# Performance work log

Measured on AMD Instinct MI355X. Metric: run time of the kernel, lower is better.

## Reference

```python
import jax, jax.numpy as jnp
from jax import lax
import numpy as np

B, P, G, C = 16, 6000, 128, 10
PC_MIN = np.array([-54.0, -54.0, -5.0], np.float32)
PC_MAX = np.array([54.0, 54.0, 3.0], np.float32)
CENTER_RADIUS = 1.5
CANDIDATE_TOPK = 5
NUM_HEADS = 6
CLS_W, ALPHA, GAMMA = 2.0, 0.25, 2.0
REG_W, IOU_W = 0.25, 0.25
EPS = 1e-12
INF1, INF2 = 10000.0, 100000.0


def _aabb(boxes):
    # boxes: (N,7) [cx,cy,cz,dx,dy,dz,yaw] -> AABB (min,max) of the 8 rotated corners
    c, d, yaw = boxes[:, :3], boxes[:, 3:6], boxes[:, 6]
    ca, sa = jnp.abs(jnp.cos(yaw)), jnp.abs(jnp.sin(yaw))
    hx = 0.5 * (d[:, 0] * ca + d[:, 1] * sa)
    hy = 0.5 * (d[:, 0] * sa + d[:, 1] * ca)
    h = jnp.stack([hx, hy, 0.5 * d[:, 2]], -1)
    return c - h, c + h


def _iou3d(pred7, gt7):
    # axis-aligned 3D IoU over corner AABBs (reference stand-in for rotated BboxOverlaps3D)
    pmin, pmax = _aabb(pred7)
    gmin, gmax = _aabb(gt7)
    lo = jnp.maximum(pmin[:, None], gmin[None])   # (P,G,3)
    hi = jnp.minimum(pmax[:, None], gmax[None])
    inter = jnp.prod(jnp.maximum(hi - lo, 0.0), -1)
    vp = jnp.prod(pmax - pmin, -1)
    vg = jnp.prod(gmax - gmin, -1)
    return inter / (vp[:, None] + vg[None] - inter + 1e-7)


def _cost_matrix(pred_logits, pred_boxes, gt_boxes, gt_labels):
    # --- focal classification cost ---
    p = jax.nn.sigmoid(pred_logits)                                  # (P,C)
    neg = -jnp.log(1.0 - p + EPS) * (1.0 - ALPHA) * p ** GAMMA
    pos = -jnp.log(p + EPS) * ALPHA * (1.0 - p) ** GAMMA
    cls_cost = (pos - neg)[:, gt_labels] * CLS_W                     # (P,G)

    gt_norm = jnp.concatenate([gt_boxes[:, :3], jnp.log(gt_boxes[:, 3:6]),
                               jnp.sin(gt_boxes[:, 6:7]), jnp.cos(gt_boxes[:, 6:7])], -1)  # (G,8)
    reg_cost = jnp.abs(pred_boxes[:, None, :8] - gt_norm[None]).sum(-1) * REG_W

    # --- IoU cost on denormalized pred boxes ---
    yaw = jnp.arctan2(pred_boxes[:, 6], pred_boxes[:, 7])
    pred7 = jnp.concatenate([pred_boxes[:, :3], jnp.exp(pred_boxes[:, 3:6]), yaw[:, None]], -1)
    ious = _iou3d(pred7, gt_boxes)                                   # (P,G)
    iou_cost = -ious * IOU_W

    # --- in-gt-box / in-center geometric prior ---
    ctr = pred_boxes[:, :3]
    gmin, gmax = _aabb(gt_boxes)
    in_box = jnp.all((ctr[:, None] > gmin[None]) & (ctr[:, None] < gmax[None]), -1)  # (P,G)
    gc, gd = gt_boxes[:, :3], gt_boxes[:, 3:6]
    lo = gc - CENTER_RADIUS * gd
    hi = gc + CENTER_RADIUS * gd
    in_ctr = jnp.all((ctr[:, None] > lo[None]) & (ctr[:, None] < hi[None]), -1)
    valid = jnp.any(in_box, 1) | jnp.any(in_ctr, 1)                  # (P,)
    in_both = in_box & in_ctr

    cost = cls_cost + reg_cost + iou_cost + (~in_both).astype(cls_cost.dtype) * 100.0
    cost = cost + (~valid).astype(cls_cost.dtype)[:, None] * INF1
    return cost, ious, valid


def _assign(pred_logits, pred_boxes, gt_boxes, gt_labels, head_idx):
    cost, ious, valid = _cost_matrix(pred_logits, pred_boxes, gt_boxes, gt_labels)

    # dynamic-k per gt: sum of top-k ious minus head-schedule offset, truncated, min 1
    k = min(CANDIDATE_TOPK, P)
    topk_ious = lax.top_k(ious.T, k)[0]                              # (G,k)
    dyn = jnp.maximum((topk_ious.sum(1) - 0.5 * (NUM_HEADS - head_idx)).astype(jnp.int32), 1)

    # per-gt lowest-cost top-dyn selection via double argsort ranks
    ranks = jnp.argsort(jnp.argsort(cost, axis=0), axis=0)           # (P,G)
    matching = (ranks < dyn[None, :]).astype(cost.dtype)

    # priors matched to >1 gt: keep only the min-cost gt
    prior_mask = matching.sum(1) > 1
    onehot_min = jax.nn.one_hot(jnp.argmin(cost, 1), G, dtype=cost.dtype)
    matching = jnp.where(prior_mask[:, None], onehot_min, matching)

    rows = jnp.arange(P)

    def cond(s):
        i, cst, m = s
        return jnp.any(m.sum(0) == 0) & (i < G + 8)

    def body(s):
        i, cst, m = s
        cst = cst + (m.sum(1) > 0).astype(cst.dtype)[:, None] * INF2
        unmatched = m.sum(0) == 0                                    # (G,)
        pos = jnp.argmin(cst, 0)                                     # (G,) best prior per gt
        m = jnp.where((rows[:, None] == pos[None]) & unmatched[None], 1.0, m)
        over = jnp.any(m.sum(1) > 1)
        oh = jax.nn.one_hot(jnp.argmin(cst, 1), G, dtype=cst.dtype)
        m = jnp.where(over & prior_mask[:, None], oh, m)             # stale mask, as in torch source
        return i + 1, cst, m

    _, _, matching = lax.while_loop(cond, body, (jnp.int32(0), cost, matching))

    fg = matching.sum(1) > 0                                         # (P,) foreground mask
    matched = jnp.where(fg, jnp.argmax(matching, 1), -1).astype(jnp.int32)
    return fg, matched


def setup_inputs():
    key = jax.random.key(0)
    k1, k2, k3, k4, k5, k6, k7, k8 = jax.random.split(key, 8)
    pred_logits = jax.random.normal(k1, (B, P, C), jnp.float32)
    ctr = jax.random.uniform(k2, (B, P, 3), jnp.float32, jnp.array(PC_MIN), jnp.array(PC_MAX))
    logsz = jnp.log(jax.random.uniform(k3, (B, P, 3), jnp.float32, 1.0, 4.0))
    ang = jax.random.uniform(k4, (B, P, 1), jnp.float32, -np.pi, np.pi)
    vel = jax.random.normal(k5, (B, P, 2), jnp.float32)
    pred_boxes = jnp.concatenate([ctr, logsz, jnp.sin(ang), jnp.cos(ang), vel], -1)
    gctr = jax.random.uniform(k6, (B, G, 3), jnp.float32, jnp.array(PC_MIN), jnp.array(PC_MAX))
    gsz = jax.random.uniform(k7, (B, G, 3), jnp.float32, 1.0, 5.0)
    gyaw = jax.random.uniform(k8, (B, G, 1), jnp.float32, -np.pi, np.pi)
    gt_boxes = jnp.concatenate([gctr, gsz, gyaw], -1)
    gt_labels = jax.random.randint(jax.random.fold_in(key, 99), (B, G), 0, C)
    return {"pred_logits": pred_logits, "pred_boxes": pred_boxes,
            "gt_boxes": gt_boxes, "gt_labels": gt_labels, "head_idx": 5}


def reference(pred_logits, pred_boxes, gt_boxes, gt_labels, head_idx):
    f = lambda pl, pb, gb, gl: _assign(pl, pb, gb, gl, head_idx)
    fg, matched = jax.vmap(f)(pred_logits, pred_boxes, gt_boxes, gt_labels)
    return fg, matched
```

## Files before the change

kernel.cpp:

```cpp
#include <hip/hip_runtime.h>
#include <stdint.h>
#include <math.h>

#define NB 16
#define NP 6000
#define NG 128
#define NC 10
#define SELMAX 4
#define GSTR 24
#define CPB 2
#define QN 24
#define EPIW 128

typedef unsigned long long u64;
#define NBPs ((size_t)NB * NP)

__device__ __forceinline__ uint32_t fkey(float f) {
  uint32_t u = __float_as_uint(f);
  return (u & 0x80000000u) ? ~u : (u | 0x80000000u);
}
__device__ __forceinline__ float fkey_inv(uint32_t k) {
  uint32_t u = (k & 0x80000000u) ? (k & 0x7fffffffu) : ~k;
  return __uint_as_float(u);
}
__device__ __forceinline__ u64 shfl_xor_u64(u64 v, int m) {
  uint32_t lo = (uint32_t)v, hi = (uint32_t)(v >> 32);
  lo = (uint32_t)__shfl_xor((int)lo, m, 64);
  hi = (uint32_t)__shfl_xor((int)hi, m, 64);
  return ((u64)hi << 32) | lo;
}
__device__ __forceinline__ u64 block_min_u64(u64 v, u64* sred, int lane, int wid) {
  for (int o = 1; o < 64; o <<= 1) {
    u64 t = shfl_xor_u64(v, o);
    if (t < v) v = t;
  }
  __syncthreads();
  if (lane == 0) sred[wid] = v;
  __syncthreads();
  u64 r = sred[0];
  if (sred[1] < r) r = sred[1];
  if (sred[2] < r) r = sred[2];
  if (sred[3] < r) r = sred[3];
  return r;
}

__device__ __forceinline__ void ins5max(uint32_t& a0, uint32_t& a1, uint32_t& a2,
                                        uint32_t& a3, uint32_t& a4, uint32_t k) {
  if (k > a4) {
    a4 = k;
    if (a4 > a3) { uint32_t t = a4; a4 = a3; a3 = t; }
    if (a3 > a2) { uint32_t t = a3; a3 = a2; a2 = t; }
    if (a2 > a1) { uint32_t t = a2; a2 = a1; a1 = t; }
    if (a1 > a0) { uint32_t t = a1; a1 = a0; a0 = t; }
  }
}
__device__ __forceinline__ void ins4min(u64& c0, u64& c1, u64& c2, u64& c3, u64 k) {
  if (k < c3) {
    c3 = k;
    if (c3 < c2) { u64 t = c3; c3 = c2; c2 = t; }
    if (c2 < c1) { u64 t = c2; c2 = c1; c1 = t; }
    if (c1 < c0) { u64 t = c1; c1 = c0; c0 = t; }
  }
}
__device__ __forceinline__ void wave_top5_iou(uint32_t a0, uint32_t a1,
                                              uint32_t a2, uint32_t a3,
                                              uint32_t a4, int lane,
                                              float* dst) {
  int hp = 0;
  for (int k = 0; k < 5; ++k) {
    uint32_t cand = (hp == 0) ? a0 : (hp == 1) ? a1 : (hp == 2) ? a2
                  : (hp == 3) ? a3 : (hp == 4) ? a4 : 0u;
    u64 key = ((u64)cand << 32) | (unsigned)lane;
    u64 r = key;
    for (int o = 1; o < 64; o <<= 1) {
      u64 t = shfl_xor_u64(r, o);
      if (t > r) r = t;
    }
    if (lane == 0) dst[k] = fkey_inv((uint32_t)(r >> 32));
    if (r == key) hp++;
  }
}
__device__ __forceinline__ void wave_top4_cost(u64 c0, u64 c1, u64 c2, u64 c3,
                                               int lane, u64* dst) {
  int hp = 0;
  for (int k = 0; k < 4; ++k) {
    u64 cand = (hp == 0) ? c0 : (hp == 1) ? c1 : (hp == 2) ? c2
             : (hp == 3) ? c3 : ~0ull;
    u64 r = cand;
    for (int o = 1; o < 64; o <<= 1) {
      u64 t = shfl_xor_u64(r, o);
      if (t < r) r = t;
    }
    if (lane == 0) dst[k] = r;
    if (r == cand) hp++;
  }
}

__global__ __launch_bounds__(256) void prep_kernel(
    const float* __restrict__ gt_boxes,
    const int* __restrict__ gt_labels,
    const float* __restrict__ pred_logits,
    const float* __restrict__ pred_boxes,
    float* __restrict__ gtaux,
    float* __restrict__ paux,
    float* __restrict__ clst,
    int* __restrict__ rowcnt,
    int* __restrict__ rowassign,
    int* __restrict__ colcnt,
    int* __restrict__ wcount) {
#pragma clang fp contract(off)
  __shared__ float shg[NG * 12];
  const int b = blockIdx.y, tid = threadIdx.x;
  if (tid < NG) {
    const int g = tid;
    const float* gb = gt_boxes + ((size_t)b * NG + g) * 7;
    float cx = gb[0], cy = gb[1], cz = gb[2];
    float dx = gb[3], dy = gb[4], dz = gb[5];
    float yaw = gb[6];
    float cyw = cosf(yaw), syw = sinf(yaw);
    float ca = fabsf(cyw), sa = fabsf(syw);
    float hx = 0.5f * (dx * ca + dy * sa);
    float hy = 0.5f * (dx * sa + dy * ca);
    float hz = 0.5f * dz;
    float gmin0 = cx - hx, gmin1 = cy - hy, gmin2 = cz - hz;
    float gmax0 = cx + hx, gmax1 = cy + hy, gmax2 = cz + hz;
    float* s = &shg[g * 12];
    s[0] = gmin0; s[1] = gmin1; s[2] = gmin2;
    s[3] = gmax0; s[4] = gmax1; s[5] = gmax2;
    s[6] = cx - 1.5f * dx; s[7] = cy - 1.5f * dy; s[8] = cz - 1.5f * dz;
    s[9] = cx + 1.5f * dx; s[10] = cy + 1.5f * dy; s[11] = cz + 1.5f * dz;
    if (blockIdx.x == 0) {
      float vg = ((gmax0 - gmin0) * (gmax1 - gmin1)) * (gmax2 - gmin2);
      float* o = gtaux + ((size_t)b * NG + g) * GSTR;
      o[0] = gmin0; o[1] = gmin1; o[2] = gmin2;
      o[3] = gmax0; o[4] = gmax1; o[5] = gmax2;
      o[6] = s[6]; o[7] = s[7]; o[8] = s[8];
      o[9] = s[9]; o[10] = s[10]; o[11] = s[11];
      o[12] = cx; o[13] = cy; o[14] = cz;
      o[15] = logf(dx); o[16] = logf(dy); o[17] = logf(dz);
      o[18] = syw; o[19] = cyw;
      o[20] = vg;
      o[21] = __int_as_float(gt_labels[(size_t)b * NG + g]);
      o[22] = 0.0f; o[23] = 0.0f;
      colcnt[b * NG + g] = 0;
      if (b == 0 && g == 0) wcount[0] = 0;
    }
  }
  __syncthreads();
  const int p = blockIdx.x * 256 + tid;
  if (p >= NP) return;
  const size_t idx = (size_t)b * NP + p;
  const float* lg = pred_logits + idx * NC;
  for (int c = 0; c < NC; ++c) {
    float x = lg[c];
    float pr = 1.0f / (1.0f + expf(-x));
    float neg = (-logf(1.0f - pr + 1e-12f) * 0.75f) * (pr * pr);
    float pos = (-logf(pr + 1e-12f) * 0.25f) * ((1.0f - pr) * (1.0f - pr));
    clst[(size_t)c * NBPs + idx] = (pos - neg) * 2.0f;
  }
  const float* bx = pred_boxes + idx * 10;
  float b0 = bx[0], b1 = bx[1], b2 = bx[2], b3 = bx[3], b4 = bx[4];
  float b5 = bx[5], b6 = bx[6], b7 = bx[7];
  float yaw = atan2f(b6, b7);
  float d0 = expf(b3), d1 = expf(b4), d2 = expf(b5);
  float ca = fabsf(cosf(yaw)), sa = fabsf(sinf(yaw));
  float hx = 0.5f * (d0 * ca + d1 * sa);
  float hy = 0.5f * (d0 * sa + d1 * ca);
  float hz = 0.5f * d2;
  float pmin0 = b0 - hx, pmin1 = b1 - hy, pmin2 = b2 - hz;
  float pmax0 = b0 + hx, pmax1 = b1 + hy, pmax2 = b2 + hz;
  int valid = 0;
  for (int g = 0; g < NG; ++g) {
    const float* s = &shg[g * 12];
    bool inb = (b0 > s[0]) && (b0 < s[3]) && (b1 > s[1]) && (b1 < s[4]) &&
               (b2 > s[2]) && (b2 < s[5]);
    bool inc = (b0 > s[6]) && (b0 < s[9]) && (b1 > s[7]) && (b1 < s[10]) &&
               (b2 > s[8]) && (b2 < s[11]);
    if (inb || inc) { valid = 1; break; }
  }
  float* o = paux + idx * 16;
  o[0] = b0; o[1] = b1; o[2] = b2; o[3] = b3;
  o[4] = b4; o[5] = b5; o[6] = b6; o[7] = b7;
  o[8] = pmin0; o[9] = pmin1; o[10] = pmin2;
  o[11] = pmax0; o[12] = pmax1; o[13] = pmax2;
  o[14] = ((pmax0 - pmin0) * (pmax1 - pmin1)) * (pmax2 - pmin2);
  o[15] = valid ? 0.0f : 10000.0f;
  rowcnt[idx] = 0;
  rowassign[idx] = 0x7fffffff;
}

struct GTp {
  float gmin0, gmin1, gmin2, gmax0, gmax1, gmax2;
  float lo0, lo1, lo2, hi0, hi1, hi2;
  float gtn0, gtn1, gtn2, gtn3, gtn4, gtn5, gtn6, gtn7;
  float vg;
  int label;
};
__device__ __forceinline__ GTp load_gt(const float* __restrict__ gtaux,
                                       int b, int g) {
  const float* ga = gtaux + ((size_t)b * NG + g) * GSTR;
  GTp t;
  t.gmin0 = ga[0]; t.gmin1 = ga[1]; t.gmin2 = ga[2];
  t.gmax0 = ga[3]; t.gmax1 = ga[4]; t.gmax2 = ga[5];
  t.lo0 = ga[6]; t.lo1 = ga[7]; t.lo2 = ga[8];
  t.hi0 = ga[9]; t.hi1 = ga[10]; t.hi2 = ga[11];
  t.gtn0 = ga[12]; t.gtn1 = ga[13]; t.gtn2 = ga[14]; t.gtn3 = ga[15];
  t.gtn4 = ga[16]; t.gtn5 = ga[17]; t.gtn6 = ga[18]; t.gtn7 = ga[19];
  t.vg = ga[20];
  t.label = __float_as_int(ga[21]);
  return t;
}

__device__ __forceinline__ float cost_base(
    float b0, float b1, float b2, float b3, float b4, float b5, float b6,
    float b7, float pmin0, float pmin1, float pmin2, float pmax0, float pmax1,
    float pmax2, float vp, float cls, const GTp& t, float* iou_out) {
#pragma clang fp contract(off)
  float r = fabsf(b0 - t.gtn0);
  r = r + fabsf(b1 - t.gtn1);
  r = r + fabsf(b2 - t.gtn2);
  r = r + fabsf(b3 - t.gtn3);
  r = r + fabsf(b4 - t.gtn4);
  r = r + fabsf(b5 - t.gtn5);
  r = r + fabsf(b6 - t.gtn6);
  r = r + fabsf(b7 - t.gtn7);
  float reg = r * 0.25f;
  float li0 = fmaxf(pmin0, t.gmin0), li1 = fmaxf(pmin1, t.gmin1),
        li2 = fmaxf(pmin2, t.gmin2);
  float hj0 = fminf(pmax0, t.gmax0), hj1 = fminf(pmax1, t.gmax1),
        hj2 = fminf(pmax2, t.gmax2);
  float e0 = fmaxf(hj0 - li0, 0.0f), e1 = fmaxf(hj1 - li1, 0.0f),
        e2 = fmaxf(hj2 - li2, 0.0f);
  float inter = (e0 * e1) * e2;
  float iou = inter / (((vp + t.vg) - inter) + 1e-7f);
  bool inb = (b0 > t.gmin0) && (b0 < t.gmax0) && (b1 > t.gmin1) &&
             (b1 < t.gmax1) && (b2 > t.gmin2) && (b2 < t.gmax2);
  bool inc = (b0 > t.lo0) && (b0 < t.hi0) && (b1 > t.lo1) && (b1 < t.hi1) &&
             (b2 > t.lo2) && (b2 < t.hi2);
  *iou_out = iou;
  return ((cls + reg) + (-(iou * 0.25f))) + ((inb && inc) ? 0.0f : 100.0f);
}

__global__ __launch_bounds__(256) void select_kernel(
    const float* __restrict__ paux,
    const float* __restrict__ clst,
    const float* __restrict__ gtaux,
    const int* __restrict__ head_ptr,
    int* __restrict__ colsel,
    int* __restrict__ rowcnt,
    int* __restrict__ rowassign,
    int* __restrict__ wlist,
    int* __restrict__ wcount) {
#pragma clang fp contract(off)
  const int n = blockIdx.x;
  const int orig = (n & 7) * 128 + (n >> 3);
  const int b = orig >> 6;
  const int g0 = (orig & 63) * CPB;
  const int tid = threadIdx.x;
  const int lane = tid & 63, wid = tid >> 6;

  const GTp t0 = load_gt(gtaux, b, g0);
  const GTp t1 = load_gt(gtaux, b, g0 + 1);
  const size_t rowbase = (size_t)b * NP;

  uint32_t i0a = 0, i0b = 0, i0c = 0, i0d = 0, i0e = 0;
  uint32_t i1a = 0, i1b = 0, i1c = 0, i1d = 0, i1e = 0;
  u64 k0a = ~0ull, k0b = ~0ull, k0c = ~0ull, k0d = ~0ull;
  u64 k1a = ~0ull, k1b = ~0ull, k1c = ~0ull, k1d = ~0ull;

  for (int q = 0; q < QN; ++q) {
    const int p = q * 256 + tid;
    if (p < NP) {
      const size_t idx = rowbase + p;
      const float4* pa = (const float4*)(paux + idx * 16);
      float4 A = pa[0], B = pa[1], C = pa[2], D = pa[3];
      float cls0 = clst[(size_t)t0.label * NBPs + idx];
      float cls1 = clst[(size_t)t1.label * NBPs + idx];
      float iou0, iou1;
      float c0 = cost_base(A.x, A.y, A.z, A.w, B.x, B.y, B.z, B.w,
                           C.x, C.y, C.z, C.w, D.x, D.y, D.z,
                           cls0, t0, &iou0);
      float c1 = cost_base(A.x, A.y, A.z, A.w, B.x, B.y, B.z, B.w,
                           C.x, C.y, C.z, C.w, D.x, D.y, D.z,
                           cls1, t1, &iou1);
      ins5max(i0a, i0b, i0c, i0d, i0e, fkey(iou0));
      ins5max(i1a, i1b, i1c, i1d, i1e, fkey(iou1));
      ins4min(k0a, k0b, k0c, k0d, ((u64)fkey(c0 + D.w) << 32) | (unsigned)p);
      ins4min(k1a, k1b, k1c, k1d, ((u64)fkey(c1 + D.w) << 32) | (unsigned)p);
    }
  }

  __shared__ float iouF[4][CPB][5];
  __shared__ u64 ckF[4][CPB][4];
  wave_top5_iou(i0a, i0b, i0c, i0d, i0e, lane, &iouF[wid][0][0]);
  wave_top5_iou(i1a, i1b, i1c, i1d, i1e, lane, &iouF[wid][1][0]);
  wave_top4_cost(k0a, k0b, k0c, k0d, lane, &ckF[wid][0][0]);
  wave_top4_cost(k1a, k1b, k1c, k1d, lane, &ckF[wid][1][0]);
  __syncthreads();

  if (tid < CPB) {
    const int c = tid;
    const int g = g0 + c;
    const int col = b * NG + g;
    float m0 = -INFINITY, m1 = -INFINITY, m2 = -INFINITY, m3 = -INFINITY,
          m4 = -INFINITY;
    for (int w = 0; w < 4; ++w) {
      for (int j = 0; j < 5; ++j) {
        float v = iouF[w][c][j];
        if (v > m4) {
          m4 = v;
          if (m4 > m3) { float t = m4; m4 = m3; m3 = t; }
          if (m3 > m2) { float t = m3; m3 = m2; m2 = t; }
          if (m2 > m1) { float t = m2; m2 = m1; m1 = t; }
          if (m1 > m0) { float t = m1; m1 = m0; m0 = t; }
        }
      }
    }
    float sum5 = ((((m0 + m1) + m2) + m3) + m4);
    float adj = sum5 - 0.5f * (float)(6 - head_ptr[0]);
    int dyn = (int)adj;
    if (dyn < 1) dyn = 1;
    if (dyn > SELMAX) dyn = SELMAX;
    u64 s0 = ~0ull, s1 = ~0ull, s2 = ~0ull, s3 = ~0ull;
    for (int w = 0; w < 4; ++w) {
      for (int j = 0; j < 4; ++j) {
        u64 k = ckF[w][c][j];
        if (k < s3) {
          s3 = k;
          if (s3 < s2) { u64 t = s3; s3 = s2; s2 = t; }
          if (s2 < s1) { u64 t = s2; s2 = s1; s1 = t; }
          if (s1 < s0) { u64 t = s1; s1 = s0; s0 = t; }
        }
      }
    }
    int pk0 = (int)(s0 & 0xffffffffu);
    int pk1 = (int)(s1 & 0xffffffffu);
    int pk2 = (int)(s2 & 0xffffffffu);
    int pk3 = (int)(s3 & 0xffffffffu);
    int sel0 = (dyn > 0) ? pk0 : -1;
    int sel1 = (dyn > 1) ? pk1 : -1;
    int sel2 = (dyn > 2) ? pk2 : -1;
    int sel3 = (dyn > 3) ? pk3 : -1;
    colsel[(size_t)col * SELMAX + 0] = sel0;
    colsel[(size_t)col * SELMAX + 1] = sel1;
    colsel[(size_t)col * SELMAX + 2] = sel2;
    colsel[(size_t)col * SELMAX + 3] = sel3;
    int sels[4] = {sel0, sel1, sel2, sel3};
    for (int k = 0; k < SELMAX; ++k) {
      int sel = sels[k];
      if (sel >= 0) {
        int old = atomicAdd(&rowcnt[rowbase + sel], 1);
        if (old == 1) {
          int slot = atomicAdd(wcount, 1);
          wlist[slot] = (int)(rowbase + sel);
        }
        atomicMin(&rowassign[rowbase + sel], g);
      }
    }
  }
}

__global__ __launch_bounds__(256) void epi_kernel(
    const float* __restrict__ paux,
    const float* __restrict__ clst,
    const float* __restrict__ gtaux,
    const int* __restrict__ colsel,
    const int* __restrict__ rowcnt,
    const int* __restrict__ wlist,
    const int* __restrict__ wcount,
    int* __restrict__ rowminArr,
    int* __restrict__ colcnt) {
#pragma clang fp contract(off)
  const int tid = threadIdx.x;
  if (blockIdx.x >= EPIW) {
    const int col = (blockIdx.x - EPIW) * 256 + tid;
    if (col < NB * NG) {
      const int b = col / NG;
      int cnt = 0;
      const size_t cb = (size_t)col * SELMAX;
      for (int k = 0; k < SELMAX; ++k) {
        int s = colsel[cb + k];
        if (s >= 0 && rowcnt[(size_t)b * NP + s] == 1) cnt++;
      }
      if (cnt) atomicAdd(&colcnt[col], cnt);
    }
    return;
  }
  const int lane = tid & 63, wid = tid >> 6;
  const int wavesTotal = EPIW * 4;
  const int wave = blockIdx.x * 4 + wid;
  const int n = wcount[0];
  for (int e = wave; e < n; e += wavesTotal) {
    const int idx = wlist[e];
    const int b = idx / NP;
    const float4* pa = (const float4*)(paux + (size_t)idx * 16);
    float4 A = pa[0], Bq = pa[1], Cq = pa[2], Dq = pa[3];
    const float pen = Dq.w;
    u64 best = ~0ull;
    for (int h = 0; h < 2; ++h) {
      const int g = h * 64 + lane;
      GTp t = load_gt(gtaux, b, g);
      float cls = clst[(size_t)t.label * NBPs + idx];
      float iou;
      float cc = cost_base(A.x, A.y, A.z, A.w, Bq.x, Bq.y, Bq.z, Bq.w,
                           Cq.x, Cq.y, Cq.z, Cq.w, Dq.x, Dq.y, Dq.z,
                           cls, t, &iou);
      u64 key = ((u64)fkey(cc + pen) << 32) | (unsigned)g;
      if (key < best) best = key;
    }
    for (int o = 1; o < 64; o <<= 1) {
      u64 t = shfl_xor_u64(best, o);
      if (t < best) best = t;
    }
    if (lane == 0) {
      const int bg = (int)(best & 0xffffffffu);
      rowminArr[idx] = bg;
      atomicAdd(&colcnt[b * NG + bg], 1);
    }
  }
}

__global__ __launch_bounds__(256) void fixup_kernel(
    const float* __restrict__ paux,
    const float* __restrict__ clst,
    const float* __restrict__ gtaux,
    const int* __restrict__ colcnt,
    const int* __restrict__ rowcnt,
    int* __restrict__ rowassign) {
#pragma clang fp contract(off)
  const int g = blockIdx.x, b = blockIdx.y, tid = threadIdx.x;
  if (colcnt[b * NG + g] != 0) return;
  const int lane = tid & 63, wid = tid >> 6;
  const size_t rowbase = (size_t)b * NP;
  GTp t = load_gt(gtaux, b, g);
  u64 best = ~0ull;
  for (int p = tid; p < NP; p += 256) {
    const size_t idx = rowbase + p;
    if (rowcnt[idx] == 0) {
      const float4* pa = (const float4*)(paux + idx * 16);
      float4 A = pa[0], Bq = pa[1], Cq = pa[2], Dq = pa[3];
      float cls = clst[(size_t)t.label * NBPs + idx];
      float iou;
      float cc = cost_base(A.x, A.y, A.z, A.w, Bq.x, Bq.y, Bq.z, Bq.w,
                           Cq.x, Cq.y, Cq.z, Cq.w, Dq.x, Dq.y, Dq.z,
                           cls, t, &iou);
      u64 key = ((u64)fkey(cc + Dq.w) << 32) | (unsigned)p;
      if (key < best) best = key;
    }
  }
  __shared__ u64 sred[4];
  u64 rr = block_min_u64(best, sred, lane, wid);
  if (tid == 0) {
    int pos = (int)(rr & 0xffffffffu);
    atomicMin(&rowassign[rowbase + pos], g);
  }
}

__global__ void output_kernel(const int* __restrict__ rowcnt,
                              const int* __restrict__ rowassign,
                              const int* __restrict__ rowminArr,
                              int* __restrict__ out) {
  const int i = blockIdx.x * 256 + threadIdx.x;
  if (i >= (int)NBPs) return;
  int rc = rowcnt[i];
  int fg, m;
  if (rc == 0) {
    int ra = rowassign[i];
    if (ra == 0x7fffffff) { fg = 0; m = -1; }
    else { fg = 1; m = ra; }
  } else if (rc == 1) {
    fg = 1; m = rowassign[i];
  } else {
    fg = 1; m = rowminArr[i];
  }
  out[i] = fg;
  out[NBPs + i] = m;
}

extern "C" void kernel_launch(void* const* d_in, const int* in_sizes, int n_in,
                              void* d_out, int out_size, void* d_ws, size_t ws_size,
                              hipStream_t stream) {
  const float* pred_logits = (const float*)d_in[0];
  const float* pred_boxes = (const float*)d_in[1];
  const float* gt_boxes = (const float*)d_in[2];
  const int* gt_labels = (const int*)d_in[3];
  const int* head = (const int*)d_in[4];
  (void)in_sizes; (void)n_in; (void)out_size; (void)ws_size;

  char* w = (char*)d_ws;
  size_t off = 0;
  auto alloc = [&](size_t bytes) -> void* {
    void* p = w + off;
    off += (bytes + 255) & ~(size_t)255;
    return p;
  };
  float* paux = (float*)alloc((size_t)NB * NP * 16 * 4);
  float* clst = (float*)alloc((size_t)NC * NB * NP * 4);
  float* gtaux = (float*)alloc((size_t)NB * NG * GSTR * 4);
  int* colsel = (int*)alloc((size_t)NB * NG * SELMAX * 4);
  int* rowcnt = (int*)alloc((size_t)NB * NP * 4);
  int* rowassign = (int*)alloc((size_t)NB * NP * 4);
  int* rowminArr = (int*)alloc((size_t)NB * NP * 4);
  int* colcnt = (int*)alloc((size_t)NB * NG * 4);
  int* wlist = (int*)alloc((size_t)NB * NP * 4);
  int* wcount = (int*)alloc(256);

  int* out = (int*)d_out;
  dim3 blk(256);
  prep_kernel<<<dim3((NP + 255) / 256, NB), blk, 0, stream>>>(
      gt_boxes, gt_labels, pred_logits, pred_boxes, gtaux, paux, clst,
      rowcnt, rowassign, colcnt, wcount);
  select_kernel<<<dim3(NB * NG / CPB), blk, 0, stream>>>(
      paux, clst, gtaux, head, colsel, rowcnt, rowassign, wlist, wcount);
  epi_kernel<<<dim3(EPIW + 8), blk, 0, stream>>>(
      paux, clst, gtaux, colsel, rowcnt, wlist, wcount, rowminArr, colcnt);
  fixup_kernel<<<dim3(NG, NB), blk, 0, stream>>>(
      paux, clst, gtaux, colcnt, rowcnt, rowassign);
  output_kernel<<<dim3(((int)NBPs + 255) / 256), blk, 0, stream>>>(
      rowcnt, rowassign, rowminArr, out);
}
```

Baseline: 117.2 us.

## Split select over prediction halves, add merge kernel, skip IoU for non-overlapping boxes

The select kernel now splits each GT column pair's 6000 predictions into two halves, doubling the block count to 2048. Per-half top-5 IoU and top-4 cost partials are written to global memory. A new merge kernel combines the partials, computes the dynamic k and performs the atomic assignment. The per-pair cost evaluation also adds an AABB overlap test that skips the IoU division and in-box checks when the boxes cannot overlap. This initialises IoU candidates to the key of 0 so zero IoUs are implied. It costs an extra kernel launch and a small global round trip, and adds divergence inside each wave.

```diff
diff --git a/kernel.cpp b/kernel.cpp
--- a/kernel.cpp
+++ b/kernel.cpp
@@ -9,7 +9,9 @@
 #define SELMAX 4
 #define GSTR 24
 #define CPB 2
-#define QN 24
+#define PS 2
+#define PPC 3000
+#define QS 12
 #define EPIW 128
 
 typedef unsigned long long u64;
@@ -241,72 +243,111 @@
   return ((cls + reg) + (-(iou * 0.25f))) + ((inb && inc) ? 0.0f : 100.0f);
 }
 
+__device__ __forceinline__ void eval_fast(
+    float b0, float b1, float b2, float b3, float b4, float b5, float b6,
+    float b7, float pmin0, float pmin1, float pmin2, float pmax0, float pmax1,
+    float pmax2, float vp, float cls, const GTp& t,
+    uint32_t& a0, uint32_t& a1, uint32_t& a2, uint32_t& a3, uint32_t& a4,
+    float* cc_out) {
+#pragma clang fp contract(off)
+  float r = fabsf(b0 - t.gtn0);
+  r = r + fabsf(b1 - t.gtn1);
+  r = r + fabsf(b2 - t.gtn2);
+  r = r + fabsf(b3 - t.gtn3);
+  r = r + fabsf(b4 - t.gtn4);
+  r = r + fabsf(b5 - t.gtn5);
+  r = r + fabsf(b6 - t.gtn6);
+  r = r + fabsf(b7 - t.gtn7);
+  float reg = r * 0.25f;
+  bool ov = (pmin0 < t.gmax0) && (pmax0 > t.gmin0) &&
+            (pmin1 < t.gmax1) && (pmax1 > t.gmin1) &&
+            (pmin2 < t.gmax2) && (pmax2 > t.gmin2);
+  float cc;
+  if (ov) {
+    float li0 = fmaxf(pmin0, t.gmin0), li1 = fmaxf(pmin1, t.gmin1),
+          li2 = fmaxf(pmin2, t.gmin2);
+    float hj0 = fminf(pmax0, t.gmax0), hj1 = fminf(pmax1, t.gmax1),
+          hj2 = fminf(pmax2, t.gmax2);
+    float e0 = fmaxf(hj0 - li0, 0.0f), e1 = fmaxf(hj1 - li1, 0.0f),
+          e2 = fmaxf(hj2 - li2, 0.0f);
+    float inter = (e0 * e1) * e2;
+    float iou = inter / (((vp + t.vg) - inter) + 1e-7f);
+    bool inb = (b0 > t.gmin0) && (b0 < t.gmax0) && (b1 > t.gmin1) &&
+               (b1 < t.gmax1) && (b2 > t.gmin2) && (b2 < t.gmax2);
+    bool inc = (b0 > t.lo0) && (b0 < t.hi0) && (b1 > t.lo1) && (b1 < t.hi1) &&
+               (b2 > t.lo2) && (b2 < t.hi2);
+    cc = ((cls + reg) + (-(iou * 0.25f))) + ((inb && inc) ? 0.0f : 100.0f);
+    ins5max(a0, a1, a2, a3, a4, fkey(iou));
+  } else {
+    cc = (cls + reg) + 100.0f;
+  }
+  *cc_out = cc;
+}
+
 __global__ __launch_bounds__(256) void select_kernel(
     const float* __restrict__ paux,
     const float* __restrict__ clst,
     const float* __restrict__ gtaux,
-    const int* __restrict__ head_ptr,
-    int* __restrict__ colsel,
-    int* __restrict__ rowcnt,
-    int* __restrict__ rowassign,
-    int* __restrict__ wlist,
-    int* __restrict__ wcount) {
+    float* __restrict__ iou5F,
+    u64* __restrict__ ckF) {
 #pragma clang fp contract(off)
   const int n = blockIdx.x;
-  const int orig = (n & 7) * 128 + (n >> 3);
-  const int b = orig >> 6;
-  const int g0 = (orig & 63) * CPB;
+  const int orig = (n & 7) * 256 + (n >> 3);
+  const int b = orig >> 7;
+  const int rem = orig & 127;
+  const int gq = rem >> 1, ps = rem & 1;
+  const int g0 = gq * CPB;
   const int tid = threadIdx.x;
   const int lane = tid & 63, wid = tid >> 6;
 
   const GTp t0 = load_gt(gtaux, b, g0);
   const GTp t1 = load_gt(gtaux, b, g0 + 1);
   const size_t rowbase = (size_t)b * NP;
-
-  uint32_t i0a = 0, i0b = 0, i0c = 0, i0d = 0, i0e = 0;
-  uint32_t i1a = 0, i1b = 0, i1c = 0, i1d = 0, i1e = 0;
+  const int pbase = ps * PPC;
+
+  const uint32_t Z = fkey(0.0f);
+  uint32_t i0a = Z, i0b = Z, i0c = Z, i0d = Z, i0e = Z;
+  uint32_t i1a = Z, i1b = Z, i1c = Z, i1d = Z, i1e = Z;
   u64 k0a = ~0ull, k0b = ~0ull, k0c = ~0ull, k0d = ~0ull;
   u64 k1a = ~0ull, k1b = ~0ull, k1c = ~0ull, k1d = ~0ull;
 
-  for (int q = 0; q < QN; ++q) {
-    const int p = q * 256 + tid;
-    if (p < NP) {
+  for (int q = 0; q < QS; ++q) {
+    const int off = q * 256 + tid;
+    if (off < PPC) {
+      const int p = pbase + off;
       const size_t idx = rowbase + p;
       const float4* pa = (const float4*)(paux + idx * 16);
       float4 A = pa[0], B = pa[1], C = pa[2], D = pa[3];
       float cls0 = clst[(size_t)t0.label * NBPs + idx];
       float cls1 = clst[(size_t)t1.label * NBPs + idx];
-      float iou0, iou1;
-      float c0 = cost_base(A.x, A.y, A.z, A.w, B.x, B.y, B.z, B.w,
-                           C.x, C.y, C.z, C.w, D.x, D.y, D.z,
-                           cls0, t0, &iou0);
-      float c1 = cost_base(A.x, A.y, A.z, A.w, B.x, B.y, B.z, B.w,
-                           C.x, C.y, C.z, C.w, D.x, D.y, D.z,
-                           cls1, t1, &iou1);
-      ins5max(i0a, i0b, i0c, i0d, i0e, fkey(iou0));
-      ins5max(i1a, i1b, i1c, i1d, i1e, fkey(iou1));
-      ins4min(k0a, k0b, k0c, k0d, ((u64)fkey(c0 + D.w) << 32) | (unsigned)p);
-      ins4min(k1a, k1b, k1c, k1d, ((u64)fkey(c1 + D.w) << 32) | (unsigned)p);
-    }
-  }
-
-  __shared__ float iouF[4][CPB][5];
-  __shared__ u64 ckF[4][CPB][4];
-  wave_top5_iou(i0a, i0b, i0c, i0d, i0e, lane, &iouF[wid][0][0]);
-  wave_top5_iou(i1a, i1b, i1c, i1d, i1e, lane, &iouF[wid][1][0]);
-  wave_top4_cost(k0a, k0b, k0c, k0d, lane, &ckF[wid][0][0]);
-  wave_top4_cost(k1a, k1b, k1c, k1d, lane, &ckF[wid][1][0]);
+      float cc0, cc1;
+      eval_fast(A.x, A.y, A.z, A.w, B.x, B.y, B.z, B.w,
+                C.x, C.y, C.z, C.w, D.x, D.y, D.z, cls0, t0,
+                i0a, i0b, i0c, i0d, i0e, &cc0);
+      eval_fast(A.x, A.y, A.z, A.w, B.x, B.y, B.z, B.w,
+                C.x, C.y, C.z, C.w, D.x, D.y, D.z, cls1, t1,
+                i1a, i1b, i1c, i1d, i1e, &cc1);
+      ins4min(k0a, k0b, k0c, k0d, ((u64)fkey(cc0 + D.w) << 32) | (unsigned)p);
+      ins4min(k1a, k1b, k1c, k1d, ((u64)fkey(cc1 + D.w) << 32) | (unsigned)p);
+    }
+  }
+
+  __shared__ float iouW[4][CPB][5];
+  __shared__ u64 ckW[4][CPB][4];
+  wave_top5_iou(i0a, i0b, i0c, i0d, i0e, lane, &iouW[wid][0][0]);
+  wave_top5_iou(i1a, i1b, i1c, i1d, i1e, lane, &iouW[wid][1][0]);
+  wave_top4_cost(k0a, k0b, k0c, k0d, lane, &ckW[wid][0][0]);
+  wave_top4_cost(k1a, k1b, k1c, k1d, lane, &ckW[wid][1][0]);
   __syncthreads();
 
   if (tid < CPB) {
     const int c = tid;
-    const int g = g0 + c;
-    const int col = b * NG + g;
+    const int col = b * NG + g0 + c;
     float m0 = -INFINITY, m1 = -INFINITY, m2 = -INFINITY, m3 = -INFINITY,
           m4 = -INFINITY;
     for (int w = 0; w < 4; ++w) {
       for (int j = 0; j < 5; ++j) {
-        float v = iouF[w][c][j];
+        float v = iouW[w][c][j];
         if (v > m4) {
           m4 = v;
           if (m4 > m3) { float t = m4; m4 = m3; m3 = t; }
@@ -316,15 +357,10 @@
         }
       }
     }
-    float sum5 = ((((m0 + m1) + m2) + m3) + m4);
-    float adj = sum5 - 0.5f * (float)(6 - head_ptr[0]);
-    int dyn = (int)adj;
-    if (dyn < 1) dyn = 1;
-    if (dyn > SELMAX) dyn = SELMAX;
     u64 s0 = ~0ull, s1 = ~0ull, s2 = ~0ull, s3 = ~0ull;
     for (int w = 0; w < 4; ++w) {
       for (int j = 0; j < 4; ++j) {
-        u64 k = ckF[w][c][j];
+        u64 k = ckW[w][c][j];
         if (k < s3) {
           s3 = k;
           if (s3 < s2) { u64 t = s3; s3 = s2; s2 = t; }
@@ -333,29 +369,72 @@
         }
       }
     }
-    int pk0 = (int)(s0 & 0xffffffffu);
-    int pk1 = (int)(s1 & 0xffffffffu);
-    int pk2 = (int)(s2 & 0xffffffffu);
-    int pk3 = (int)(s3 & 0xffffffffu);
-    int sel0 = (dyn > 0) ? pk0 : -1;
-    int sel1 = (dyn > 1) ? pk1 : -1;
-    int sel2 = (dyn > 2) ? pk2 : -1;
-    int sel3 = (dyn > 3) ? pk3 : -1;
-    colsel[(size_t)col * SELMAX + 0] = sel0;
-    colsel[(size_t)col * SELMAX + 1] = sel1;
-    colsel[(size_t)col * SELMAX + 2] = sel2;
-    colsel[(size_t)col * SELMAX + 3] = sel3;
-    int sels[4] = {sel0, sel1, sel2, sel3};
-    for (int k = 0; k < SELMAX; ++k) {
-      int sel = sels[k];
-      if (sel >= 0) {
-        int old = atomicAdd(&rowcnt[rowbase + sel], 1);
-        if (old == 1) {
-          int slot = atomicAdd(wcount, 1);
-          wlist[slot] = (int)(rowbase + sel);
-        }
-        atomicMin(&rowassign[rowbase + sel], g);
+    float* fi = iou5F + (size_t)col * (PS * 5) + ps * 5;
+    fi[0] = m0; fi[1] = m1; fi[2] = m2; fi[3] = m3; fi[4] = m4;
+    u64* fc = ckF + (size_t)col * (PS * 4) + ps * 4;
+    fc[0] = s0; fc[1] = s1; fc[2] = s2; fc[3] = s3;
+  }
+}
+
+__global__ __launch_bounds__(256) void merge_kernel(
+    const float* __restrict__ iou5F,
+    const u64* __restrict__ ckF,
+    const int* __restrict__ head_ptr,
+    int* __restrict__ colsel,
+    int* __restrict__ rowcnt,
+    int* __restrict__ rowassign,
+    int* __restrict__ wlist,
+    int* __restrict__ wcount) {
+#pragma clang fp contract(off)
+  const int col = blockIdx.x * 256 + threadIdx.x;
+  if (col >= NB * NG) return;
+  const int b = col / NG, g = col - b * NG;
+  const float* ip = iou5F + (size_t)col * (PS * 5);
+  float m0 = -INFINITY, m1 = -INFINITY, m2 = -INFINITY, m3 = -INFINITY,
+        m4 = -INFINITY;
+  for (int i = 0; i < PS * 5; ++i) {
+    float v = ip[i];
+    if (v > m4) {
+      m4 = v;
+      if (m4 > m3) { float t = m4; m4 = m3; m3 = t; }
+      if (m3 > m2) { float t = m3; m3 = m2; m2 = t; }
+      if (m2 > m1) { float t = m2; m2 = m1; m1 = t; }
+      if (m1 > m0) { float t = m1; m1 = m0; m0 = t; }
+    }
+  }
+  float sum5 = ((((m0 + m1) + m2) + m3) + m4);
+  float adj = sum5 - 0.5f * (float)(6 - head_ptr[0]);
+  int dyn = (int)adj;
+  if (dyn < 1) dyn = 1;
+  if (dyn > SELMAX) dyn = SELMAX;
+
+  const u64* kp = ckF + (size_t)col * (PS * 4);
+  u64 s0 = ~0ull, s1 = ~0ull, s2 = ~0ull, s3 = ~0ull;
+  for (int i = 0; i < PS * 4; ++i) {
+    u64 k = kp[i];
+    if (k < s3) {
+      s3 = k;
+      if (s3 < s2) { u64 t = s3; s3 = s2; s2 = t; }
+      if (s2 < s1) { u64 t = s2; s2 = s1; s1 = t; }
+      if (s1 < s0) { u64 t = s1; s1 = s0; s0 = t; }
+    }
+  }
+  const size_t rowbase = (size_t)b * NP;
+  int pk[4];
+  pk[0] = (int)(s0 & 0xffffffffu);
+  pk[1] = (int)(s1 & 0xffffffffu);
+  pk[2] = (int)(s2 & 0xffffffffu);
+  pk[3] = (int)(s3 & 0xffffffffu);
+  for (int k = 0; k < SELMAX; ++k) {
+    int sel = (k < dyn) ? pk[k] : -1;
+    colsel[(size_t)col * SELMAX + k] = sel;
+    if (sel >= 0) {
+      int old = atomicAdd(&rowcnt[rowbase + sel], 1);
+      if (old == 1) {
+        int slot = atomicAdd(wcount, 1);
+        wlist[slot] = (int)(rowbase + sel);
       }
+      atomicMin(&rowassign[rowbase + sel], g);
     }
   }
 }
@@ -497,6 +576,8 @@
   float* paux = (float*)alloc((size_t)NB * NP * 16 * 4);
   float* clst = (float*)alloc((size_t)NC * NB * NP * 4);
   float* gtaux = (float*)alloc((size_t)NB * NG * GSTR * 4);
+  float* iou5F = (float*)alloc((size_t)NB * NG * PS * 5 * 4);
+  u64* ckF = (u64*)alloc((size_t)NB * NG * PS * 4 * 8);
   int* colsel = (int*)alloc((size_t)NB * NG * SELMAX * 4);
   int* rowcnt = (int*)alloc((size_t)NB * NP * 4);
   int* rowassign = (int*)alloc((size_t)NB * NP * 4);
@@ -510,8 +591,10 @@
   prep_kernel<<<dim3((NP + 255) / 256, NB), blk, 0, stream>>>(
       gt_boxes, gt_labels, pred_logits, pred_boxes, gtaux, paux, clst,
       rowcnt, rowassign, colcnt, wcount);
-  select_kernel<<<dim3(NB * NG / CPB), blk, 0, stream>>>(
-      paux, clst, gtaux, head, colsel, rowcnt, rowassign, wlist, wcount);
+  select_kernel<<<dim3(NB * (NG / CPB) * PS), blk, 0, stream>>>(
+      paux, clst, gtaux, iou5F, ckF);
+  merge_kernel<<<dim3((NB * NG + 255) / 256), blk, 0, stream>>>(
+      iou5F, ckF, head, colsel, rowcnt, rowassign, wlist, wcount);
   epi_kernel<<<dim3(EPIW + 8), blk, 0, stream>>>(
       paux, clst, gtaux, colsel, rowcnt, wlist, wcount, rowminArr, colcnt);
   fixup_kernel<<<dim3(NG, NB), blk, 0, stream>>>(
```

After: 118.6 us. No clear change (+1.2%).
